# Kernel tuning notes

Hardware: AMD Instinct MI355X
Metric: run time of the kernel (lower is better)

Reference implementation:

```python
import jax, jax.numpy as jnp
import numpy as np

N = 50000      # nodes
E = 1600000    # edges (avg degree 32)
D_IN = 128
HID = 64


def setup_inputs() -> dict:
    key = jax.random.key(0)
    ks = jax.random.split(key, 7)
    x = jax.random.normal(ks[0], (N, D_IN), dtype=jnp.float32)
    ei = jax.random.randint(ks[1], (2, E), 0, N, dtype=jnp.int32)
    ew = jax.random.uniform(ks[2], (E,), dtype=jnp.float32)
    # GCNConv linear weights (glorot-ish scale); lin has no bias, conv bias added post-aggregation
    W1 = jax.random.normal(ks[3], (HID, D_IN), dtype=jnp.float32) * (1.0 / np.sqrt(D_IN))
    b1 = jnp.zeros((HID,), dtype=jnp.float32)
    W2 = jax.random.normal(ks[4], (HID, HID), dtype=jnp.float32) * (1.0 / np.sqrt(HID))
    b2 = jnp.zeros((HID,), dtype=jnp.float32)
    return {"x": x, "ei": ei, "ew": ew, "W1": W1, "b1": b1, "W2": W2, "b2": b2}


def _gcn_conv(x, src, dst, ew_all, W, b, n_nodes):
    """PyG GCNConv: gcn_norm (self-loops already appended) + x@W.T, gather-scale-scatter, +b."""
    deg = jax.ops.segment_sum(ew_all, dst, num_segments=n_nodes)  # dst-side weighted degree
    dinv = jnp.where(deg > 0, jax.lax.rsqrt(deg), 0.0)            # deg^{-1/2}, inf->0
    norm = dinv[src] * ew_all * dinv[dst]                          # [E+N]
    h = x @ W.T                                                    # [N, hid]
    msg = h[src] * norm[:, None]                                   # gather + scale
    out = jax.ops.segment_sum(msg, dst, num_segments=n_nodes)     # scatter-add
    return out + b


def reference(x, ei, ew, W1, b1, W2, b2):
    n_nodes = x.shape[0]
    # add self loops once (fill value 1.0), shared by both conv layers
    loop = jnp.arange(n_nodes, dtype=ei.dtype)
    src = jnp.concatenate([ei[0], loop])
    dst = jnp.concatenate([ei[1], loop])
    ew_all = jnp.concatenate([ew, jnp.ones((n_nodes,), dtype=ew.dtype)])

    h1 = jax.nn.relu(_gcn_conv(x, src, dst, ew_all, W1, b1, n_nodes))
    # dropout is identity in eval mode
    h2 = _gcn_conv(h1, src, dst, ew_all, W2, b2, n_nodes)
    return h2 + h1
```

## Files before the change

kernel.cpp:

```cpp
#include <hip/hip_runtime.h>

#define HID 64
#define DIN 128
#define NBLK 512

typedef unsigned long long ull;
typedef unsigned short u16;

static __device__ __forceinline__ u16 f2bf(float f) {
  unsigned u = __float_as_uint(f);
  unsigned lsb = (u >> 16) & 1u;
  u += 0x7fffu + lsb;
  return (u16)(u >> 16);
}


__global__ __launch_bounds__(512) void k_histA(const int* __restrict__ dst,
                                               int* __restrict__ G,
                                               int E, int NBC, int chunk) {
  __shared__ int h[256];
  int b = blockIdx.x, tid = threadIdx.x;
  if (tid < 256) h[tid] = 0;
  __syncthreads();
  int e0 = b * chunk, e1 = min(E, e0 + chunk);
  for (int e = e0 + tid; e < e1; e += 512) atomicAdd(&h[dst[e] >> 8], 1);
  __syncthreads();
  if (tid < NBC) G[tid * NBLK + b] = h[tid];
}


__global__ __launch_bounds__(256) void k_chunksum(const int* __restrict__ G, int* bsum, int L) {
  int b = blockIdx.x, t = threadIdx.x;
  int base = b * 2048;
  int s = 0;
  for (int i = t; i < 2048; i += 256) {
    int g = base + i;
    s += (g < L) ? G[g] : 0;
  }
  __shared__ int red[4];
  for (int o = 32; o > 0; o >>= 1) s += __shfl_down(s, o);
  if ((t & 63) == 0) red[t >> 6] = s;
  __syncthreads();
  if (t == 0) bsum[b] = red[0] + red[1] + red[2] + red[3];
}

__global__ __launch_bounds__(64) void k_scanbsum(int* bsum, int nb) {
  int lane = threadIdx.x;
  int v = (lane < nb) ? bsum[lane] : 0;
  int incl = v;
  for (int o = 1; o < 64; o <<= 1) {
    int u = __shfl_up(incl, o);
    if (lane >= o) incl += u;
  }
  if (lane < nb) bsum[lane] = incl - v;
}

__global__ __launch_bounds__(256) void k_scanfinal(int* G, const int* __restrict__ bsum, int L) {
  int b = blockIdx.x, t = threadIdx.x;
  int i0 = b * 2048 + t * 8;
  int v[8], tsum = 0;
#pragma unroll
  for (int k = 0; k < 8; ++k) {
    v[k] = (i0 + k < L) ? G[i0 + k] : 0;
    tsum += v[k];
  }
  int incl = tsum;
  for (int o = 1; o < 64; o <<= 1) {
    int u = __shfl_up(incl, o);
    if ((t & 63) >= o) incl += u;
  }
  int wexcl = incl - tsum;
  __shared__ int wtot[4];
  int w = t >> 6;
  if ((t & 63) == 63) wtot[w] = incl;
  __syncthreads();
  int wbase = 0;
  for (int i = 0; i < w; ++i) wbase += wtot[i];
  int run = bsum[b] + wbase + wexcl;
#pragma unroll
  for (int k = 0; k < 8; ++k) {
    if (i0 + k < L) G[i0 + k] = run;
    run += v[k];
  }
}


__global__ __launch_bounds__(512) void k_scatterA(const int* __restrict__ src,
                                                  const int* __restrict__ dst,
                                                  const float* __restrict__ ew,
                                                  const int* __restrict__ Gs,
                                                  int2* __restrict__ bufA,
                                                  int E, int NBC, int chunk) {
  __shared__ int cur[256];
  int b = blockIdx.x, tid = threadIdx.x;
  if (tid < NBC) cur[tid] = Gs[tid * NBLK + b];
  __syncthreads();
  int e0 = b * chunk, e1 = min(E, e0 + chunk);
  for (int e = e0 + tid; e < e1; e += 512) {
    int s = src[e], d = dst[e];
    float w = ew[e];
    int p = atomicAdd(&cur[d >> 8], 1);
    bufA[p] = make_int2(__float_as_int(w), (int)(((unsigned)s << 16) | (unsigned)d));
  }
}


__global__ __launch_bounds__(512) void k_passB(const int2* __restrict__ bufA,
                                               const int* __restrict__ Gs,
                                               int2* __restrict__ bufB,
                                               int* __restrict__ offs,
                                               float* __restrict__ dinv,
                                               int NBC, int E, int N) {
  int bin = blockIdx.x, tid = threadIdx.x;
  __shared__ int h2[256];
  __shared__ int cur[256];
  __shared__ float dg[256];
  int base = Gs[bin * NBLK];
  int end  = (bin + 1 < NBC) ? Gs[(bin + 1) * NBLK] : E;
  int m = end - base;
  if (tid < 256) { h2[tid] = 0; dg[tid] = 0.f; }
  __syncthreads();
  for (int i = tid; i < m; i += 512) {
    unsigned sd = (unsigned)bufA[base + i].y;
    atomicAdd(&h2[sd & 255], 1);
  }
  __syncthreads();
  int own = (tid < 256) ? h2[tid] : 0;
  for (int o = 1; o < 256; o <<= 1) {
    int u = 0;
    if (tid < 256 && tid >= o) u = h2[tid - o];
    __syncthreads();
    if (tid < 256) h2[tid] += u;
    __syncthreads();
  }
  int nd = (bin << 8) + tid;
  if (tid < 256) {
    int excl = h2[tid] - own;
    cur[tid] = excl;
    if (nd < N) offs[nd] = base + excl;
  }
  if (bin == NBC - 1 && tid == 0) offs[N] = E;
  __syncthreads();
  for (int i = tid; i < m; i += 512) {
    int2 r = bufA[base + i];
    unsigned sd = (unsigned)r.y;
    int dl = (int)(sd & 255u);
    int p = atomicAdd(&cur[dl], 1);
    bufB[base + p] = r;
    atomicAdd(&dg[dl], __int_as_float(r.x));
  }
  __syncthreads();
  if (tid < 256 && nd < N) dinv[nd] = rsqrtf(1.0f + dg[tid]);
}


__global__ __launch_bounds__(256) void k_norm(int2* __restrict__ recs,
                                              const float* __restrict__ dinv, int E) {
  int e = blockIdx.x * 256 + threadIdx.x;
  if (e < E) {
    int2 r = recs[e];
    unsigned sd = (unsigned)r.y;
    int s = (int)(sd >> 16), d = (int)(sd & 0xffffu);
    float nrm = dinv[s] * __int_as_float(r.x) * dinv[d];
    recs[e] = make_int2(__float_as_int(nrm), s);
  }
}


__global__ __launch_bounds__(256) void k_transW2(const float* __restrict__ W1,
                                                 const float* __restrict__ W2,
                                                 float* __restrict__ WT1,
                                                 float* __restrict__ WT2) {
  int idx = blockIdx.x * 256 + threadIdx.x;
  if (idx < DIN * 64) {
    int d = idx >> 6, j = idx & 63;
    WT1[idx] = W1[j * DIN + d];
  }
  int i2 = idx - DIN * 64;
  if (i2 >= 0 && i2 < HID * 64) {
    int d = i2 >> 6, j = i2 & 63;
    WT2[i2] = W2[j * HID + d];
  }
}


template <int K>
__global__ __launch_bounds__(256) void k_gemm(const float* __restrict__ X,
                                              const float* __restrict__ WTg,
                                              u16* __restrict__ out, int n_nodes) {
  constexpr int PAD = 68;
  __shared__ float XT[64 * PAD];
  __shared__ float WL[64 * PAD];
  const int tid = threadIdx.x;
  const int n0 = blockIdx.x * 64;
  const int tx = tid & 15;
  const int ty = tid >> 4;
  float acc[4][4] = {{0.f}};

  for (int ph = 0; ph < K / 64; ++ph) {
    const int d0 = ph * 64;
    __syncthreads();
#pragma unroll
    for (int k = 0; k < 4; ++k) {
      int f = tid + k * 256;
      int r = f >> 4, q = f & 15;
      int n = n0 + r;
      float4 xv = (n < n_nodes)
        ? *reinterpret_cast<const float4*>(&X[(size_t)n * K + d0 + 4 * q])
        : make_float4(0.f, 0.f, 0.f, 0.f);
      *reinterpret_cast<float4*>(&XT[r * PAD + 4 * q]) = xv;
      float4 wv = *reinterpret_cast<const float4*>(&WTg[(size_t)(d0 + r) * 64 + 4 * q]);
      *reinterpret_cast<float4*>(&WL[r * PAD + 4 * q]) = wv;
    }
    __syncthreads();
#pragma unroll 4
    for (int dd = 0; dd < 64; dd += 4) {
      float4 xs[4], ws[4];
#pragma unroll
      for (int mi = 0; mi < 4; ++mi)
        xs[mi] = *reinterpret_cast<const float4*>(&XT[(4 * ty + mi) * PAD + dd]);
#pragma unroll
      for (int dk = 0; dk < 4; ++dk)
        ws[dk] = *reinterpret_cast<const float4*>(&WL[(dd + dk) * PAD + 4 * tx]);
#pragma unroll
      for (int mi = 0; mi < 4; ++mi) {
        float xm[4] = {xs[mi].x, xs[mi].y, xs[mi].z, xs[mi].w};
#pragma unroll
        for (int dk = 0; dk < 4; ++dk) {
          acc[mi][0] = fmaf(xm[dk], ws[dk].x, acc[mi][0]);
          acc[mi][1] = fmaf(xm[dk], ws[dk].y, acc[mi][1]);
          acc[mi][2] = fmaf(xm[dk], ws[dk].z, acc[mi][2]);
          acc[mi][3] = fmaf(xm[dk], ws[dk].w, acc[mi][3]);
        }
      }
    }
  }

#pragma unroll
  for (int mi = 0; mi < 4; ++mi) {
    int n = n0 + 4 * ty + mi;
    if (n < n_nodes) {
      ushort4 o = make_ushort4(f2bf(acc[mi][0]), f2bf(acc[mi][1]),
                               f2bf(acc[mi][2]), f2bf(acc[mi][3]));
      *reinterpret_cast<ushort4*>(&out[(size_t)n * HID + 4 * tx]) = o;
    }
  }
}


__device__ __forceinline__ void bfma(uint2 v, float w,
                                     float& a0, float& a1, float& a2, float& a3) {
  a0 = fmaf(__uint_as_float(v.x << 16), w, a0);
  a1 = fmaf(__uint_as_float(v.x & 0xffff0000u), w, a1);
  a2 = fmaf(__uint_as_float(v.y << 16), w, a2);
  a3 = fmaf(__uint_as_float(v.y & 0xffff0000u), w, a3);
}

__global__ __launch_bounds__(256) void k_agg(const u16* __restrict__ h,
                                             const int2* __restrict__ recs,
                                             const int* __restrict__ offs,
                                             const float* __restrict__ dinv,
                                             const float* __restrict__ bias,
                                             const float* __restrict__ resid,
                                             float* __restrict__ out, int n_nodes, int mode) {
  int tid = threadIdx.x;
  int lane = tid & 63;
  int q = lane >> 4;
  int p4 = (lane & 15) * 4;
  int node = (blockIdx.x * 4 + (tid >> 6)) * 4 + q;
  if (node >= n_nodes) return;
  int beg = offs[node], end = offs[node + 1];
  float di = dinv[node];

  float a0, a1, a2, a3;
  float b0 = 0.f, b1 = 0.f, b2 = 0.f, b3 = 0.f;
  {
    uint2 v = *reinterpret_cast<const uint2*>(&h[(size_t)node * HID + p4]);
    float w = di * di;
    a0 = __uint_as_float(v.x << 16) * w;
    a1 = __uint_as_float(v.x & 0xffff0000u) * w;
    a2 = __uint_as_float(v.y << 16) * w;
    a3 = __uint_as_float(v.y & 0xffff0000u) * w;
  }

  int i = beg;
  while (i + 8 <= end) {
    int2 r0 = recs[i];     int2 r1 = recs[i + 1];
    int2 r2 = recs[i + 2]; int2 r3 = recs[i + 3];
    int2 r4 = recs[i + 4]; int2 r5 = recs[i + 5];
    int2 r6 = recs[i + 6]; int2 r7 = recs[i + 7];
    uint2 v0 = *reinterpret_cast<const uint2*>(&h[(size_t)r0.y * HID + p4]);
    uint2 v1 = *reinterpret_cast<const uint2*>(&h[(size_t)r1.y * HID + p4]);
    uint2 v2 = *reinterpret_cast<const uint2*>(&h[(size_t)r2.y * HID + p4]);
    uint2 v3 = *reinterpret_cast<const uint2*>(&h[(size_t)r3.y * HID + p4]);
    uint2 v4 = *reinterpret_cast<const uint2*>(&h[(size_t)r4.y * HID + p4]);
    uint2 v5 = *reinterpret_cast<const uint2*>(&h[(size_t)r5.y * HID + p4]);
    uint2 v6 = *reinterpret_cast<const uint2*>(&h[(size_t)r6.y * HID + p4]);
    uint2 v7 = *reinterpret_cast<const uint2*>(&h[(size_t)r7.y * HID + p4]);
    bfma(v0, __int_as_float(r0.x), a0, a1, a2, a3);
    bfma(v1, __int_as_float(r1.x), b0, b1, b2, b3);
    bfma(v2, __int_as_float(r2.x), a0, a1, a2, a3);
    bfma(v3, __int_as_float(r3.x), b0, b1, b2, b3);
    bfma(v4, __int_as_float(r4.x), a0, a1, a2, a3);
    bfma(v5, __int_as_float(r5.x), b0, b1, b2, b3);
    bfma(v6, __int_as_float(r6.x), a0, a1, a2, a3);
    bfma(v7, __int_as_float(r7.x), b0, b1, b2, b3);
    i += 8;
  }
  if (i + 4 <= end) {
    int2 r0 = recs[i];     int2 r1 = recs[i + 1];
    int2 r2 = recs[i + 2]; int2 r3 = recs[i + 3];
    uint2 v0 = *reinterpret_cast<const uint2*>(&h[(size_t)r0.y * HID + p4]);
    uint2 v1 = *reinterpret_cast<const uint2*>(&h[(size_t)r1.y * HID + p4]);
    uint2 v2 = *reinterpret_cast<const uint2*>(&h[(size_t)r2.y * HID + p4]);
    uint2 v3 = *reinterpret_cast<const uint2*>(&h[(size_t)r3.y * HID + p4]);
    bfma(v0, __int_as_float(r0.x), a0, a1, a2, a3);
    bfma(v1, __int_as_float(r1.x), b0, b1, b2, b3);
    bfma(v2, __int_as_float(r2.x), a0, a1, a2, a3);
    bfma(v3, __int_as_float(r3.x), b0, b1, b2, b3);
    i += 4;
  }
  if (i + 2 <= end) {
    int2 r0 = recs[i];     int2 r1 = recs[i + 1];
    uint2 v0 = *reinterpret_cast<const uint2*>(&h[(size_t)r0.y * HID + p4]);
    uint2 v1 = *reinterpret_cast<const uint2*>(&h[(size_t)r1.y * HID + p4]);
    bfma(v0, __int_as_float(r0.x), a0, a1, a2, a3);
    bfma(v1, __int_as_float(r1.x), b0, b1, b2, b3);
    i += 2;
  }
  if (i < end) {
    int2 r0 = recs[i];
    uint2 v0 = *reinterpret_cast<const uint2*>(&h[(size_t)r0.y * HID + p4]);
    bfma(v0, __int_as_float(r0.x), a0, a1, a2, a3);
  }

  float r0 = a0 + b0, r1 = a1 + b1, r2 = a2 + b2, r3 = a3 + b3;
  float4 bb = *reinterpret_cast<const float4*>(&bias[p4]);
  r0 += bb.x; r1 += bb.y; r2 += bb.z; r3 += bb.w;
  if (mode == 0) {
    r0 = fmaxf(r0, 0.f); r1 = fmaxf(r1, 0.f);
    r2 = fmaxf(r2, 0.f); r3 = fmaxf(r3, 0.f);
  } else {
    float4 rs = *reinterpret_cast<const float4*>(&resid[(size_t)node * HID + p4]);
    r0 += rs.x; r1 += rs.y; r2 += rs.z; r3 += rs.w;
  }
  *reinterpret_cast<float4*>(&out[(size_t)node * HID + p4]) = make_float4(r0, r1, r2, r3);
}


extern "C" void kernel_launch(void* const* d_in, const int* in_sizes, int n_in,
                              void* d_out, int out_size, void* d_ws, size_t ws_size,
                              hipStream_t stream) {
  const float* x  = (const float*)d_in[0];
  const int*   ei = (const int*)d_in[1];
  const float* ew = (const float*)d_in[2];
  const float* W1 = (const float*)d_in[3];
  const float* b1 = (const float*)d_in[4];
  const float* W2 = (const float*)d_in[5];
  const float* b2 = (const float*)d_in[6];
  float* out = (float*)d_out;

  const int N = in_sizes[0] / DIN;
  const int E = in_sizes[2];
  const int* src = ei;
  const int* dst = ei + E;

  const int NBC = (N + 255) >> 8;
  const int L = NBC * NBLK;
  const int chunk = (E + NBLK - 1) / NBLK;
  const int nch = (L + 2047) / 2048;

  char* p = (char*)d_ws;
  auto carve = [&](size_t bytes) {
    char* r = p;
    p += (bytes + 255) & ~(size_t)255;
    return r;
  };
  int*   G     = (int*)carve((size_t)L * 4);
  int*   bsum  = (int*)carve(64 * 4);
  int*   offs  = (int*)carve((size_t)(N + 1) * 4);
  float* dinv  = (float*)carve((size_t)N * 4);
  int2*  bufA  = (int2*)carve((size_t)E * 8);
  int2*  bufB  = (int2*)carve((size_t)E * 8);
  u16*   h     = (u16*)carve((size_t)N * HID * 2);
  float* h1    = (float*)carve((size_t)N * HID * 4);
  float* WT1   = (float*)carve((size_t)DIN * HID * 4);
  float* WT2   = (float*)carve((size_t)HID * HID * 4);

  int gblk = (N + 63) / 64;
  int ablk = (N + 15) / 16;

  k_histA<<<NBLK, 512, 0, stream>>>(dst, G, E, NBC, chunk);
  k_transW2<<<((DIN + HID) * 64 + 255) / 256, 256, 0, stream>>>(W1, W2, WT1, WT2);
  k_chunksum<<<nch, 256, 0, stream>>>(G, bsum, L);
  k_scanbsum<<<1, 64, 0, stream>>>(bsum, nch);
  k_scanfinal<<<nch, 256, 0, stream>>>(G, bsum, L);
  k_scatterA<<<NBLK, 512, 0, stream>>>(src, dst, ew, G, bufA, E, NBC, chunk);
  k_passB<<<NBC, 512, 0, stream>>>(bufA, G, bufB, offs, dinv, NBC, E, N);
  k_norm<<<(E + 255) / 256, 256, 0, stream>>>(bufB, dinv, E);

  k_gemm<DIN><<<gblk, 256, 0, stream>>>(x, WT1, h, N);
  k_agg<<<ablk, 256, 0, stream>>>(h, bufB, offs, dinv, b1, nullptr, h1, N, 0);
  k_gemm<HID><<<gblk, 256, 0, stream>>>(h1, WT2, h, N);
  k_agg<<<ablk, 256, 0, stream>>>(h, bufB, offs, dinv, b2, h1, out, N, 1);
}
```

Before: 233.1 us.

## Split bf16 feature table into two 32-column planes, aggregate each plane separately

The GEMM now writes its bf16 output as two column-half planes of 32 features, each 3.2 MB, in place of one 64-wide table. The aggregation kernel runs twice per layer, once per plane, so the random gathers hit a smaller working set that fits better in cache. The main loop is also unrolled to 16 edges. In exchange the CSR records and offsets are read twice per layer, there are two extra launches, and each gather moves 4 bytes per lane instead of 8.

```diff
diff --git a/kernel.cpp b/kernel.cpp
--- a/kernel.cpp
+++ b/kernel.cpp
@@ -187,7 +187,8 @@
 template <int K>
 __global__ __launch_bounds__(256) void k_gemm(const float* __restrict__ X,
                                               const float* __restrict__ WTg,
-                                              u16* __restrict__ out, int n_nodes) {
+                                              u16* __restrict__ h0,
+                                              u16* __restrict__ h1, int n_nodes) {
   constexpr int PAD = 68;
   __shared__ float XT[64 * PAD];
   __shared__ float WL[64 * PAD];
@@ -236,115 +237,155 @@
     }
   }
 
+  u16* plane = (tx < 8) ? h0 : h1;
+  const int col = (4 * tx) & 31;
 #pragma unroll
   for (int mi = 0; mi < 4; ++mi) {
     int n = n0 + 4 * ty + mi;
     if (n < n_nodes) {
       ushort4 o = make_ushort4(f2bf(acc[mi][0]), f2bf(acc[mi][1]),
                                f2bf(acc[mi][2]), f2bf(acc[mi][3]));
-      *reinterpret_cast<ushort4*>(&out[(size_t)n * HID + 4 * tx]) = o;
+      *reinterpret_cast<ushort4*>(&plane[(size_t)n * 32 + col]) = o;
     }
   }
 }
 
 
-__device__ __forceinline__ void bfma(uint2 v, float w,
-                                     float& a0, float& a1, float& a2, float& a3) {
-  a0 = fmaf(__uint_as_float(v.x << 16), w, a0);
-  a1 = fmaf(__uint_as_float(v.x & 0xffff0000u), w, a1);
-  a2 = fmaf(__uint_as_float(v.y << 16), w, a2);
-  a3 = fmaf(__uint_as_float(v.y & 0xffff0000u), w, a3);
-}
-
-__global__ __launch_bounds__(256) void k_agg(const u16* __restrict__ h,
-                                             const int2* __restrict__ recs,
-                                             const int* __restrict__ offs,
-                                             const float* __restrict__ dinv,
-                                             const float* __restrict__ bias,
-                                             const float* __restrict__ resid,
-                                             float* __restrict__ out, int n_nodes, int mode) {
+__device__ __forceinline__ void bfma2(unsigned v, float w, float& a0, float& a1) {
+  a0 = fmaf(__uint_as_float(v << 16), w, a0);
+  a1 = fmaf(__uint_as_float(v & 0xffff0000u), w, a1);
+}
+
+__global__ __launch_bounds__(256) void k_aggp(const u16* __restrict__ hp,
+                                              const int2* __restrict__ recs,
+                                              const int* __restrict__ offs,
+                                              const float* __restrict__ dinv,
+                                              const float* __restrict__ bias,
+                                              const float* __restrict__ resid,
+                                              float* __restrict__ out,
+                                              int n_nodes, int mode, int fbase) {
   int tid = threadIdx.x;
   int lane = tid & 63;
   int q = lane >> 4;
-  int p4 = (lane & 15) * 4;
+  int p2 = (lane & 15) * 2;
   int node = (blockIdx.x * 4 + (tid >> 6)) * 4 + q;
   if (node >= n_nodes) return;
   int beg = offs[node], end = offs[node + 1];
   float di = dinv[node];
 
-  float a0, a1, a2, a3;
-  float b0 = 0.f, b1 = 0.f, b2 = 0.f, b3 = 0.f;
+  float a0, a1;
+  float b0 = 0.f, b1 = 0.f;
   {
-    uint2 v = *reinterpret_cast<const uint2*>(&h[(size_t)node * HID + p4]);
+    unsigned v = *reinterpret_cast<const unsigned*>(&hp[(size_t)node * 32 + p2]);
     float w = di * di;
-    a0 = __uint_as_float(v.x << 16) * w;
-    a1 = __uint_as_float(v.x & 0xffff0000u) * w;
-    a2 = __uint_as_float(v.y << 16) * w;
-    a3 = __uint_as_float(v.y & 0xffff0000u) * w;
+    a0 = __uint_as_float(v << 16) * w;
+    a1 = __uint_as_float(v & 0xffff0000u) * w;
   }
 
   int i = beg;
-  while (i + 8 <= end) {
+  while (i + 16 <= end) {
+    int2 r0 = recs[i];      int2 r1 = recs[i + 1];
+    int2 r2 = recs[i + 2];  int2 r3 = recs[i + 3];
+    int2 r4 = recs[i + 4];  int2 r5 = recs[i + 5];
+    int2 r6 = recs[i + 6];  int2 r7 = recs[i + 7];
+    int2 r8 = recs[i + 8];  int2 r9 = recs[i + 9];
+    int2 rA = recs[i + 10]; int2 rB = recs[i + 11];
+    int2 rC = recs[i + 12]; int2 rD = recs[i + 13];
+    int2 rE = recs[i + 14]; int2 rF = recs[i + 15];
+    unsigned v0 = *reinterpret_cast<const unsigned*>(&hp[(size_t)r0.y * 32 + p2]);
+    unsigned v1 = *reinterpret_cast<const unsigned*>(&hp[(size_t)r1.y * 32 + p2]);
+    unsigned v2 = *reinterpret_cast<const unsigned*>(&hp[(size_t)r2.y * 32 + p2]);
+    unsigned v3 = *reinterpret_cast<const unsigned*>(&hp[(size_t)r3.y * 32 + p2]);
+    unsigned v4 = *reinterpret_cast<const unsigned*>(&hp[(size_t)r4.y * 32 + p2]);
+    unsigned v5 = *reinterpret_cast<const unsigned*>(&hp[(size_t)r5.y * 32 + p2]);
+    unsigned v6 = *reinterpret_cast<const unsigned*>(&hp[(size_t)r6.y * 32 + p2]);
+    unsigned v7 = *reinterpret_cast<const unsigned*>(&hp[(size_t)r7.y * 32 + p2]);
+    unsigned v8 = *reinterpret_cast<const unsigned*>(&hp[(size_t)r8.y * 32 + p2]);
+    unsigned v9 = *reinterpret_cast<const unsigned*>(&hp[(size_t)r9.y * 32 + p2]);
+    unsigned vA = *reinterpret_cast<const unsigned*>(&hp[(size_t)rA.y * 32 + p2]);
+    unsigned vB = *reinterpret_cast<const unsigned*>(&hp[(size_t)rB.y * 32 + p2]);
+    unsigned vC = *reinterpret_cast<const unsigned*>(&hp[(size_t)rC.y * 32 + p2]);
+    unsigned vD = *reinterpret_cast<const unsigned*>(&hp[(size_t)rD.y * 32 + p2]);
+    unsigned vE = *reinterpret_cast<const unsigned*>(&hp[(size_t)rE.y * 32 + p2]);
+    unsigned vF = *reinterpret_cast<const unsigned*>(&hp[(size_t)rF.y * 32 + p2]);
+    bfma2(v0, __int_as_float(r0.x), a0, a1);
+    bfma2(v1, __int_as_float(r1.x), b0, b1);
+    bfma2(v2, __int_as_float(r2.x), a0, a1);
+    bfma2(v3, __int_as_float(r3.x), b0, b1);
+    bfma2(v4, __int_as_float(r4.x), a0, a1);
+    bfma2(v5, __int_as_float(r5.x), b0, b1);
+    bfma2(v6, __int_as_float(r6.x), a0, a1);
+    bfma2(v7, __int_as_float(r7.x), b0, b1);
+    bfma2(v8, __int_as_float(r8.x), a0, a1);
+    bfma2(v9, __int_as_float(r9.x), b0, b1);
+    bfma2(vA, __int_as_float(rA.x), a0, a1);
+    bfma2(vB, __int_as_float(rB.x), b0, b1);
+    bfma2(vC, __int_as_float(rC.x), a0, a1);
+    bfma2(vD, __int_as_float(rD.x), b0, b1);
+    bfma2(vE, __int_as_float(rE.x), a0, a1);
+    bfma2(vF, __int_as_float(rF.x), b0, b1);
+    i += 16;
+  }
+  if (i + 8 <= end) {
     int2 r0 = recs[i];     int2 r1 = recs[i + 1];
     int2 r2 = recs[i + 2]; int2 r3 = recs[i + 3];
     int2 r4 = recs[i + 4]; int2 r5 = recs[i + 5];
     int2 r6 = recs[i + 6]; int2 r7 = recs[i + 7];
-    uint2 v0 = *reinterpret_cast<const uint2*>(&h[(size_t)r0.y * HID + p4]);
-    uint2 v1 = *reinterpret_cast<const uint2*>(&h[(size_t)r1.y * HID + p4]);
-    uint2 v2 = *reinterpret_cast<const uint2*>(&h[(size_t)r2.y * HID + p4]);
-    uint2 v3 = *reinterpret_cast<const uint2*>(&h[(size_t)r3.y * HID + p4]);
-    uint2 v4 = *reinterpret_cast<const uint2*>(&h[(size_t)r4.y * HID + p4]);
-    uint2 v5 = *reinterpret_cast<const uint2*>(&h[(size_t)r5.y * HID + p4]);
-    uint2 v6 = *reinterpret_cast<const uint2*>(&h[(size_t)r6.y * HID + p4]);
-    uint2 v7 = *reinterpret_cast<const uint2*>(&h[(size_t)r7.y * HID + p4]);
-    bfma(v0, __int_as_float(r0.x), a0, a1, a2, a3);
-    bfma(v1, __int_as_float(r1.x), b0, b1, b2, b3);
-    bfma(v2, __int_as_float(r2.x), a0, a1, a2, a3);
-    bfma(v3, __int_as_float(r3.x), b0, b1, b2, b3);
-    bfma(v4, __int_as_float(r4.x), a0, a1, a2, a3);
-    bfma(v5, __int_as_float(r5.x), b0, b1, b2, b3);
-    bfma(v6, __int_as_float(r6.x), a0, a1, a2, a3);
-    bfma(v7, __int_as_float(r7.x), b0, b1, b2, b3);
+    unsigned v0 = *reinterpret_cast<const unsigned*>(&hp[(size_t)r0.y * 32 + p2]);
+    unsigned v1 = *reinterpret_cast<const unsigned*>(&hp[(size_t)r1.y * 32 + p2]);
+    unsigned v2 = *reinterpret_cast<const unsigned*>(&hp[(size_t)r2.y * 32 + p2]);
+    unsigned v3 = *reinterpret_cast<const unsigned*>(&hp[(size_t)r3.y * 32 + p2]);
+    unsigned v4 = *reinterpret_cast<const unsigned*>(&hp[(size_t)r4.y * 32 + p2]);
+    unsigned v5 = *reinterpret_cast<const unsigned*>(&hp[(size_t)r5.y * 32 + p2]);
+    unsigned v6 = *reinterpret_cast<const unsigned*>(&hp[(size_t)r6.y * 32 + p2]);
+    unsigned v7 = *reinterpret_cast<const unsigned*>(&hp[(size_t)r7.y * 32 + p2]);
+    bfma2(v0, __int_as_float(r0.x), a0, a1);
+    bfma2(v1, __int_as_float(r1.x), b0, b1);
+    bfma2(v2, __int_as_float(r2.x), a0, a1);
+    bfma2(v3, __int_as_float(r3.x), b0, b1);
+    bfma2(v4, __int_as_float(r4.x), a0, a1);
+    bfma2(v5, __int_as_float(r5.x), b0, b1);
+    bfma2(v6, __int_as_float(r6.x), a0, a1);
+    bfma2(v7, __int_as_float(r7.x), b0, b1);
     i += 8;
   }
   if (i + 4 <= end) {
     int2 r0 = recs[i];     int2 r1 = recs[i + 1];
     int2 r2 = recs[i + 2]; int2 r3 = recs[i + 3];
-    uint2 v0 = *reinterpret_cast<const uint2*>(&h[(size_t)r0.y * HID + p4]);
-    uint2 v1 = *reinterpret_cast<const uint2*>(&h[(size_t)r1.y * HID + p4]);
-    uint2 v2 = *reinterpret_cast<const uint2*>(&h[(size_t)r2.y * HID + p4]);
-    uint2 v3 = *reinterpret_cast<const uint2*>(&h[(size_t)r3.y * HID + p4]);
-    bfma(v0, __int_as_float(r0.x), a0, a1, a2, a3);
-    bfma(v1, __int_as_float(r1.x), b0, b1, b2, b3);
-    bfma(v2, __int_as_float(r2.x), a0, a1, a2, a3);
-    bfma(v3, __int_as_float(r3.x), b0, b1, b2, b3);
+    unsigned v0 = *reinterpret_cast<const unsigned*>(&hp[(size_t)r0.y * 32 + p2]);
+    unsigned v1 = *reinterpret_cast<const unsigned*>(&hp[(size_t)r1.y * 32 + p2]);
+    unsigned v2 = *reinterpret_cast<const unsigned*>(&hp[(size_t)r2.y * 32 + p2]);
+    unsigned v3 = *reinterpret_cast<const unsigned*>(&hp[(size_t)r3.y * 32 + p2]);
+    bfma2(v0, __int_as_float(r0.x), a0, a1);
+    bfma2(v1, __int_as_float(r1.x), b0, b1);
+    bfma2(v2, __int_as_float(r2.x), a0, a1);
+    bfma2(v3, __int_as_float(r3.x), b0, b1);
     i += 4;
   }
   if (i + 2 <= end) {
     int2 r0 = recs[i];     int2 r1 = recs[i + 1];
-    uint2 v0 = *reinterpret_cast<const uint2*>(&h[(size_t)r0.y * HID + p4]);
-    uint2 v1 = *reinterpret_cast<const uint2*>(&h[(size_t)r1.y * HID + p4]);
-    bfma(v0, __int_as_float(r0.x), a0, a1, a2, a3);
-    bfma(v1, __int_as_float(r1.x), b0, b1, b2, b3);
+    unsigned v0 = *reinterpret_cast<const unsigned*>(&hp[(size_t)r0.y * 32 + p2]);
+    unsigned v1 = *reinterpret_cast<const unsigned*>(&hp[(size_t)r1.y * 32 + p2]);
+    bfma2(v0, __int_as_float(r0.x), a0, a1);
+    bfma2(v1, __int_as_float(r1.x), b0, b1);
     i += 2;
   }
   if (i < end) {
     int2 r0 = recs[i];
-    uint2 v0 = *reinterpret_cast<const uint2*>(&h[(size_t)r0.y * HID + p4]);
-    bfma(v0, __int_as_float(r0.x), a0, a1, a2, a3);
-  }
-
-  float r0 = a0 + b0, r1 = a1 + b1, r2 = a2 + b2, r3 = a3 + b3;
-  float4 bb = *reinterpret_cast<const float4*>(&bias[p4]);
-  r0 += bb.x; r1 += bb.y; r2 += bb.z; r3 += bb.w;
+    unsigned v0 = *reinterpret_cast<const unsigned*>(&hp[(size_t)r0.y * 32 + p2]);
+    bfma2(v0, __int_as_float(r0.x), a0, a1);
+  }
+
+  float r0 = a0 + b0, r1 = a1 + b1;
+  float2 bb = *reinterpret_cast<const float2*>(&bias[fbase + p2]);
+  r0 += bb.x; r1 += bb.y;
   if (mode == 0) {
     r0 = fmaxf(r0, 0.f); r1 = fmaxf(r1, 0.f);
-    r2 = fmaxf(r2, 0.f); r3 = fmaxf(r3, 0.f);
   } else {
-    float4 rs = *reinterpret_cast<const float4*>(&resid[(size_t)node * HID + p4]);
-    r0 += rs.x; r1 += rs.y; r2 += rs.z; r3 += rs.w;
-  }
-  *reinterpret_cast<float4*>(&out[(size_t)node * HID + p4]) = make_float4(r0, r1, r2, r3);
+    float2 rs = *reinterpret_cast<const float2*>(&resid[(size_t)node * HID + fbase + p2]);
+    r0 += rs.x; r1 += rs.y;
+  }
+  *reinterpret_cast<float2*>(&out[(size_t)node * HID + fbase + p2]) = make_float2(r0, r1);
 }
 
 
@@ -382,7 +423,8 @@
   float* dinv  = (float*)carve((size_t)N * 4);
   int2*  bufA  = (int2*)carve((size_t)E * 8);
   int2*  bufB  = (int2*)carve((size_t)E * 8);
-  u16*   h     = (u16*)carve((size_t)N * HID * 2);
+  u16*   h0    = (u16*)carve((size_t)N * 32 * 2);
+  u16*   h1p   = (u16*)carve((size_t)N * 32 * 2);
   float* h1    = (float*)carve((size_t)N * HID * 4);
   float* WT1   = (float*)carve((size_t)DIN * HID * 4);
   float* WT2   = (float*)carve((size_t)HID * HID * 4);
@@ -399,8 +441,10 @@
   k_passB<<<NBC, 512, 0, stream>>>(bufA, G, bufB, offs, dinv, NBC, E, N);
   k_norm<<<(E + 255) / 256, 256, 0, stream>>>(bufB, dinv, E);
 
-  k_gemm<DIN><<<gblk, 256, 0, stream>>>(x, WT1, h, N);
-  k_agg<<<ablk, 256, 0, stream>>>(h, bufB, offs, dinv, b1, nullptr, h1, N, 0);
-  k_gemm<HID><<<gblk, 256, 0, stream>>>(h1, WT2, h, N);
-  k_agg<<<ablk, 256, 0, stream>>>(h, bufB, offs, dinv, b2, h1, out, N, 1);
-}
+  k_gemm<DIN><<<gblk, 256, 0, stream>>>(x, WT1, h0, h1p, N);
+  k_aggp<<<ablk, 256, 0, stream>>>(h0,  bufB, offs, dinv, b1, nullptr, h1, N, 0, 0);
+  k_aggp<<<ablk, 256, 0, stream>>>(h1p, bufB, offs, dinv, b1, nullptr, h1, N, 0, 32);
+  k_gemm<HID><<<gblk, 256, 0, stream>>>(h1, WT2, h0, h1p, N);
+  k_aggp<<<ablk, 256, 0, stream>>>(h0,  bufB, offs, dinv, b2, h1, out, N, 1, 0);
+  k_aggp<<<ablk, 256, 0, stream>>>(h1p, bufB, offs, dinv, b2, h1, out, N, 1, 32);
+}
```

Result: slower. 260.1 us (+11.6%).

## Widen aggregation gathers to 16-byte loads and fold weight transpose into histogram

Applied to the files above, without the earlier changes.

The aggregation kernel now assigns 8 lanes per node with 8 bf16 features each, using 128-bit gathers instead of 64-bit. This doubles the nodes per wavefront and halves the number of gather instructions per edge, which should improve memory-level parallelism. The weight-transpose kernel is merged into the histogram kernel as extra blocks, saving one launch. In exchange, each thread keeps twice as many accumulator registers.

```diff
diff --git a/kernel.cpp b/kernel.cpp
--- a/kernel.cpp
+++ b/kernel.cpp
@@ -17,9 +17,26 @@
 
 __global__ __launch_bounds__(512) void k_histA(const int* __restrict__ dst,
                                                int* __restrict__ G,
-                                               int E, int NBC, int chunk) {
+                                               int E, int NBC, int chunk,
+                                               const float* __restrict__ W1,
+                                               const float* __restrict__ W2,
+                                               float* __restrict__ WT1,
+                                               float* __restrict__ WT2) {
+  int b = blockIdx.x, tid = threadIdx.x;
+  if (b >= NBLK) {
+    int idx = (b - NBLK) * 512 + tid;
+    if (idx < DIN * 64) {
+      int d = idx >> 6, j = idx & 63;
+      WT1[idx] = W1[j * DIN + d];
+    }
+    int i2 = idx - DIN * 64;
+    if (i2 >= 0 && i2 < HID * 64) {
+      int d = i2 >> 6, j = i2 & 63;
+      WT2[i2] = W2[j * HID + d];
+    }
+    return;
+  }
   __shared__ int h[256];
-  int b = blockIdx.x, tid = threadIdx.x;
   if (tid < 256) h[tid] = 0;
   __syncthreads();
   int e0 = b * chunk, e1 = min(E, e0 + chunk);
@@ -163,23 +180,6 @@
     int s = (int)(sd >> 16), d = (int)(sd & 0xffffu);
     float nrm = dinv[s] * __int_as_float(r.x) * dinv[d];
     recs[e] = make_int2(__float_as_int(nrm), s);
-  }
-}
-
-
-__global__ __launch_bounds__(256) void k_transW2(const float* __restrict__ W1,
-                                                 const float* __restrict__ W2,
-                                                 float* __restrict__ WT1,
-                                                 float* __restrict__ WT2) {
-  int idx = blockIdx.x * 256 + threadIdx.x;
-  if (idx < DIN * 64) {
-    int d = idx >> 6, j = idx & 63;
-    WT1[idx] = W1[j * DIN + d];
-  }
-  int i2 = idx - DIN * 64;
-  if (i2 >= 0 && i2 < HID * 64) {
-    int d = i2 >> 6, j = i2 & 63;
-    WT2[i2] = W2[j * HID + d];
   }
 }
 
@@ -248,12 +248,15 @@
 }
 
 
-__device__ __forceinline__ void bfma(uint2 v, float w,
-                                     float& a0, float& a1, float& a2, float& a3) {
-  a0 = fmaf(__uint_as_float(v.x << 16), w, a0);
-  a1 = fmaf(__uint_as_float(v.x & 0xffff0000u), w, a1);
-  a2 = fmaf(__uint_as_float(v.y << 16), w, a2);
-  a3 = fmaf(__uint_as_float(v.y & 0xffff0000u), w, a3);
+__device__ __forceinline__ void bfma8(const uint4& v, float w, float* a) {
+  a[0] = fmaf(__uint_as_float(v.x << 16), w, a[0]);
+  a[1] = fmaf(__uint_as_float(v.x & 0xffff0000u), w, a[1]);
+  a[2] = fmaf(__uint_as_float(v.y << 16), w, a[2]);
+  a[3] = fmaf(__uint_as_float(v.y & 0xffff0000u), w, a[3]);
+  a[4] = fmaf(__uint_as_float(v.z << 16), w, a[4]);
+  a[5] = fmaf(__uint_as_float(v.z & 0xffff0000u), w, a[5]);
+  a[6] = fmaf(__uint_as_float(v.w << 16), w, a[6]);
+  a[7] = fmaf(__uint_as_float(v.w & 0xffff0000u), w, a[7]);
 }
 
 __global__ __launch_bounds__(256) void k_agg(const u16* __restrict__ h,
@@ -265,22 +268,27 @@
                                              float* __restrict__ out, int n_nodes, int mode) {
   int tid = threadIdx.x;
   int lane = tid & 63;
-  int q = lane >> 4;
-  int p4 = (lane & 15) * 4;
-  int node = (blockIdx.x * 4 + (tid >> 6)) * 4 + q;
+  int g = lane >> 3;
+  int p8 = (lane & 7) * 8;
+  int node = (blockIdx.x * 4 + (tid >> 6)) * 8 + g;
   if (node >= n_nodes) return;
   int beg = offs[node], end = offs[node + 1];
   float di = dinv[node];
 
-  float a0, a1, a2, a3;
-  float b0 = 0.f, b1 = 0.f, b2 = 0.f, b3 = 0.f;
+  float a[8], b[8];
   {
-    uint2 v = *reinterpret_cast<const uint2*>(&h[(size_t)node * HID + p4]);
+    uint4 v = *reinterpret_cast<const uint4*>(&h[(size_t)node * HID + p8]);
     float w = di * di;
-    a0 = __uint_as_float(v.x << 16) * w;
-    a1 = __uint_as_float(v.x & 0xffff0000u) * w;
-    a2 = __uint_as_float(v.y << 16) * w;
-    a3 = __uint_as_float(v.y & 0xffff0000u) * w;
+    a[0] = __uint_as_float(v.x << 16) * w;
+    a[1] = __uint_as_float(v.x & 0xffff0000u) * w;
+    a[2] = __uint_as_float(v.y << 16) * w;
+    a[3] = __uint_as_float(v.y & 0xffff0000u) * w;
+    a[4] = __uint_as_float(v.z << 16) * w;
+    a[5] = __uint_as_float(v.z & 0xffff0000u) * w;
+    a[6] = __uint_as_float(v.w << 16) * w;
+    a[7] = __uint_as_float(v.w & 0xffff0000u) * w;
+#pragma unroll
+    for (int j = 0; j < 8; ++j) b[j] = 0.f;
   }
 
   int i = beg;
@@ -289,62 +297,71 @@
     int2 r2 = recs[i + 2]; int2 r3 = recs[i + 3];
     int2 r4 = recs[i + 4]; int2 r5 = recs[i + 5];
     int2 r6 = recs[i + 6]; int2 r7 = recs[i + 7];
-    uint2 v0 = *reinterpret_cast<const uint2*>(&h[(size_t)r0.y * HID + p4]);
-    uint2 v1 = *reinterpret_cast<const uint2*>(&h[(size_t)r1.y * HID + p4]);
-    uint2 v2 = *reinterpret_cast<const uint2*>(&h[(size_t)r2.y * HID + p4]);
-    uint2 v3 = *reinterpret_cast<const uint2*>(&h[(size_t)r3.y * HID + p4]);
-    uint2 v4 = *reinterpret_cast<const uint2*>(&h[(size_t)r4.y * HID + p4]);
-    uint2 v5 = *reinterpret_cast<const uint2*>(&h[(size_t)r5.y * HID + p4]);
-    uint2 v6 = *reinterpret_cast<const uint2*>(&h[(size_t)r6.y * HID + p4]);
-    uint2 v7 = *reinterpret_cast<const uint2*>(&h[(size_t)r7.y * HID + p4]);
-    bfma(v0, __int_as_float(r0.x), a0, a1, a2, a3);
-    bfma(v1, __int_as_float(r1.x), b0, b1, b2, b3);
-    bfma(v2, __int_as_float(r2.x), a0, a1, a2, a3);
-    bfma(v3, __int_as_float(r3.x), b0, b1, b2, b3);
-    bfma(v4, __int_as_float(r4.x), a0, a1, a2, a3);
-    bfma(v5, __int_as_float(r5.x), b0, b1, b2, b3);
-    bfma(v6, __int_as_float(r6.x), a0, a1, a2, a3);
-    bfma(v7, __int_as_float(r7.x), b0, b1, b2, b3);
+    uint4 v0 = *reinterpret_cast<const uint4*>(&h[(size_t)r0.y * HID + p8]);
+    uint4 v1 = *reinterpret_cast<const uint4*>(&h[(size_t)r1.y * HID + p8]);
+    uint4 v2 = *reinterpret_cast<const uint4*>(&h[(size_t)r2.y * HID + p8]);
+    uint4 v3 = *reinterpret_cast<const uint4*>(&h[(size_t)r3.y * HID + p8]);
+    uint4 v4 = *reinterpret_cast<const uint4*>(&h[(size_t)r4.y * HID + p8]);
+    uint4 v5 = *reinterpret_cast<const uint4*>(&h[(size_t)r5.y * HID + p8]);
+    uint4 v6 = *reinterpret_cast<const uint4*>(&h[(size_t)r6.y * HID + p8]);
+    uint4 v7 = *reinterpret_cast<const uint4*>(&h[(size_t)r7.y * HID + p8]);
+    bfma8(v0, __int_as_float(r0.x), a);
+    bfma8(v1, __int_as_float(r1.x), b);
+    bfma8(v2, __int_as_float(r2.x), a);
+    bfma8(v3, __int_as_float(r3.x), b);
+    bfma8(v4, __int_as_float(r4.x), a);
+    bfma8(v5, __int_as_float(r5.x), b);
+    bfma8(v6, __int_as_float(r6.x), a);
+    bfma8(v7, __int_as_float(r7.x), b);
     i += 8;
   }
   if (i + 4 <= end) {
     int2 r0 = recs[i];     int2 r1 = recs[i + 1];
     int2 r2 = recs[i + 2]; int2 r3 = recs[i + 3];
-    uint2 v0 = *reinterpret_cast<const uint2*>(&h[(size_t)r0.y * HID + p4]);
-    uint2 v1 = *reinterpret_cast<const uint2*>(&h[(size_t)r1.y * HID + p4]);
-    uint2 v2 = *reinterpret_cast<const uint2*>(&h[(size_t)r2.y * HID + p4]);
-    uint2 v3 = *reinterpret_cast<const uint2*>(&h[(size_t)r3.y * HID + p4]);
-    bfma(v0, __int_as_float(r0.x), a0, a1, a2, a3);
-    bfma(v1, __int_as_float(r1.x), b0, b1, b2, b3);
-    bfma(v2, __int_as_float(r2.x), a0, a1, a2, a3);
-    bfma(v3, __int_as_float(r3.x), b0, b1, b2, b3);
+    uint4 v0 = *reinterpret_cast<const uint4*>(&h[(size_t)r0.y * HID + p8]);
+    uint4 v1 = *reinterpret_cast<const uint4*>(&h[(size_t)r1.y * HID + p8]);
+    uint4 v2 = *reinterpret_cast<const uint4*>(&h[(size_t)r2.y * HID + p8]);
+    uint4 v3 = *reinterpret_cast<const uint4*>(&h[(size_t)r3.y * HID + p8]);
+    bfma8(v0, __int_as_float(r0.x), a);
+    bfma8(v1, __int_as_float(r1.x), b);
+    bfma8(v2, __int_as_float(r2.x), a);
+    bfma8(v3, __int_as_float(r3.x), b);
     i += 4;
   }
   if (i + 2 <= end) {
     int2 r0 = recs[i];     int2 r1 = recs[i + 1];
-    uint2 v0 = *reinterpret_cast<const uint2*>(&h[(size_t)r0.y * HID + p4]);
-    uint2 v1 = *reinterpret_cast<const uint2*>(&h[(size_t)r1.y * HID + p4]);
-    bfma(v0, __int_as_float(r0.x), a0, a1, a2, a3);
-    bfma(v1, __int_as_float(r1.x), b0, b1, b2, b3);
+    uint4 v0 = *reinterpret_cast<const uint4*>(&h[(size_t)r0.y * HID + p8]);
+    uint4 v1 = *reinterpret_cast<const uint4*>(&h[(size_t)r1.y * HID + p8]);
+    bfma8(v0, __int_as_float(r0.x), a);
+    bfma8(v1, __int_as_float(r1.x), b);
     i += 2;
   }
   if (i < end) {
     int2 r0 = recs[i];
-    uint2 v0 = *reinterpret_cast<const uint2*>(&h[(size_t)r0.y * HID + p4]);
-    bfma(v0, __int_as_float(r0.x), a0, a1, a2, a3);
-  }
-
-  float r0 = a0 + b0, r1 = a1 + b1, r2 = a2 + b2, r3 = a3 + b3;
-  float4 bb = *reinterpret_cast<const float4*>(&bias[p4]);
-  r0 += bb.x; r1 += bb.y; r2 += bb.z; r3 += bb.w;
+    uint4 v0 = *reinterpret_cast<const uint4*>(&h[(size_t)r0.y * HID + p8]);
+    bfma8(v0, __int_as_float(r0.x), a);
+  }
+
+  float r[8];
+#pragma unroll
+  for (int j = 0; j < 8; ++j) r[j] = a[j] + b[j];
+  float4 bb0 = *reinterpret_cast<const float4*>(&bias[p8]);
+  float4 bb1 = *reinterpret_cast<const float4*>(&bias[p8 + 4]);
+  r[0] += bb0.x; r[1] += bb0.y; r[2] += bb0.z; r[3] += bb0.w;
+  r[4] += bb1.x; r[5] += bb1.y; r[6] += bb1.z; r[7] += bb1.w;
   if (mode == 0) {
-    r0 = fmaxf(r0, 0.f); r1 = fmaxf(r1, 0.f);
-    r2 = fmaxf(r2, 0.f); r3 = fmaxf(r3, 0.f);
+#pragma unroll
+    for (int j = 0; j < 8; ++j) r[j] = fmaxf(r[j], 0.f);
   } else {
-    float4 rs = *reinterpret_cast<const float4*>(&resid[(size_t)node * HID + p4]);
-    r0 += rs.x; r1 += rs.y; r2 += rs.z; r3 += rs.w;
-  }
-  *reinterpret_cast<float4*>(&out[(size_t)node * HID + p4]) = make_float4(r0, r1, r2, r3);
+    float4 rs0 = *reinterpret_cast<const float4*>(&resid[(size_t)node * HID + p8]);
+    float4 rs1 = *reinterpret_cast<const float4*>(&resid[(size_t)node * HID + p8 + 4]);
+    r[0] += rs0.x; r[1] += rs0.y; r[2] += rs0.z; r[3] += rs0.w;
+    r[4] += rs1.x; r[5] += rs1.y; r[6] += rs1.z; r[7] += rs1.w;
+  }
+  *reinterpret_cast<float4*>(&out[(size_t)node * HID + p8]) =
+      make_float4(r[0], r[1], r[2], r[3]);
+  *reinterpret_cast<float4*>(&out[(size_t)node * HID + p8 + 4]) =
+      make_float4(r[4], r[5], r[6], r[7]);
 }
 
 
@@ -388,10 +405,10 @@
   float* WT2   = (float*)carve((size_t)HID * HID * 4);
 
   int gblk = (N + 63) / 64;
-  int ablk = (N + 15) / 16;
-
-  k_histA<<<NBLK, 512, 0, stream>>>(dst, G, E, NBC, chunk);
-  k_transW2<<<((DIN + HID) * 64 + 255) / 256, 256, 0, stream>>>(W1, W2, WT1, WT2);
+  int ablk = (N + 31) / 32;
+  int tblk = ((DIN + HID) * 64 + 511) / 512;
+
+  k_histA<<<NBLK + tblk, 512, 0, stream>>>(dst, G, E, NBC, chunk, W1, W2, WT1, WT2);
   k_chunksum<<<nch, 256, 0, stream>>>(G, bsum, L);
   k_scanbsum<<<1, 64, 0, stream>>>(bsum, nch);
   k_scanfinal<<<nch, 256, 0, stream>>>(G, bsum, L);
```

Result: no change. 229.2 us (-1.6%).
